# Kernel tuning notes

Measured on AMD Instinct MI355X. Metric: run time of the kernel, lower is better.

## Reference

```python
import jax, jax.numpy as jnp
from jax import lax
import numpy as np

# pywt.Wavelet('sym5').dec_lo; true convolution with rec_lo == correlation with dec_lo
_DEC_LO = jnp.array([0.027333068345077982, 0.029519490925774643, -0.039134249302383094,
                     0.1993975339773936, 0.7234076904024206, 0.6339789634582119,
                     0.01660210576452232, -0.17532808990845047, -0.021101834024758855,
                     0.019538882735286728], dtype=jnp.float32)
_KERNEL = _DEC_LO[None, None, :]  # (O=1, I=1, L=10)


def _idwt_approx(c):
    # One inverse-DWT level with zero detail coeffs.
    # pywt idwt: upsample by 2, full conv with rec_lo, slice [L-2 : L-2 + 2n-L+2].
    # Equivalent: lhs_dilation=2, padding=(1,1), correlation with dec_lo.
    B, n = c.shape
    out = lax.conv_general_dilated(c[:, None, :], _KERNEL, window_strides=(1,),
                                   padding=[(1, 1)], lhs_dilation=(2,),
                                   dimension_numbers=('NCH', 'OIH', 'NCH'))
    return out[:, 0, :]  # (B, 2n - 8)


def _waverec3(cA):
    # waverec with coeffs [cA(20), zeros(20), zeros(31), zeros(54)], sym5 -> length 100
    a = _idwt_approx(cA)      # 20 -> 32
    a = a[:, :31]             # pywt waverec crops a to len(d)=31
    a = _idwt_approx(a)       # 31 -> 54
    a = _idwt_approx(a)       # 54 -> 100
    return a


def _ce(logits, target):
    logp = jax.nn.log_softmax(logits, axis=-1)
    return -jnp.take_along_axis(logp, target[:, None], axis=-1)[:, 0]


def _ohem(logits, target, train_mask, ratio=3.0):
    ce = _ce(logits, target)
    tf = target.astype(jnp.float32)
    pos = (tf * train_mask) > 0
    neg = ((1.0 - tf) * train_mask) > 0
    n_pos = jnp.sum(pos.astype(jnp.float32))
    count_neg = jnp.sum(neg.astype(jnp.float32))
    loss_pos = jnp.where(n_pos > 0, jnp.sum(jnp.where(pos, ce, 0.0)), 0.0)
    n_neg = jnp.where(n_pos > 0, jnp.minimum(count_neg, jnp.floor(ratio * n_pos)), 100.0)
    srt = jnp.sort(jnp.where(neg, ce, -jnp.inf))[::-1]
    take = (jnp.arange(srt.shape[0]) < n_neg) & jnp.isfinite(srt)
    loss_neg = jnp.sum(jnp.where(take, srt, 0.0))
    return (loss_pos + loss_neg) / (n_pos + n_neg)


def _smooth_l1(d):
    ad = jnp.abs(d)
    return jnp.where(ad < 1.0, 0.5 * d * d, ad - 0.5)


def _forward_single(cls_pred, reg_pred, gt):
    cp = jnp.transpose(cls_pred, (0, 2, 3, 1)).reshape(-1, 4)
    rp = jnp.transpose(reg_pred, (0, 2, 3, 1)).reshape(-1, 42)
    g = jnp.transpose(gt, (0, 2, 3, 1)).reshape(-1, 45)
    tr_pred, tcl_pred = cp[:, :2], cp[:, 2:]
    wl_r, xc_p, wl_i, yc_p = rp[:, :20], rp[:, 20], rp[:, 21:41], rp[:, 41]
    tr_mask, tcl_mask, train_mask = g[:, 0], g[:, 1], g[:, 2]
    real_g, xc_g, imag_g, yc_g = g[:, 3:23], g[:, 23], g[:, 24:44], g[:, 44]
    ttm = train_mask * tr_mask
    n_pos = jnp.sum(ttm)

    loss_tr = _ohem(tr_pred, tr_mask.astype(jnp.int32), train_mask)

    ce_tcl = _ce(tcl_pred, tcl_mask.astype(jnp.int32))
    neg_m = 1.0 - ttm
    mp = jnp.sum(ce_tcl * ttm) / jnp.maximum(n_pos, 1.0)
    mn = jnp.sum(ce_tcl * neg_m) / jnp.maximum(jnp.sum(neg_m), 1.0)
    loss_tcl = jnp.where(n_pos > 0, mp + 0.5 * mn, 0.0)

    px = _waverec3(wl_r) + xc_p[:, None]   # (M,100)
    py = _waverec3(wl_i) + yc_p[:, None]
    gx = _waverec3(real_g) + xc_g[:, None]
    gy = _waverec3(imag_g) + yc_g[:, None]
    per_pix = jnp.sum(_smooth_l1(px - gx) + _smooth_l1(py - gy), axis=-1)  # (M,)
    loss_contour = jnp.where(n_pos > 0, 0.5 * jnp.sum(ttm * per_pix) / (n_pos * 200.0), 0.0)
    return jnp.stack([loss_tr, loss_tcl, loss_contour])


def setup_inputs() -> dict:
    key = jax.random.key(0)
    N = 8
    out = {}
    for name, H in (("3", 100), ("4", 50), ("5", 25)):
        k1, k2, k3, k4, k5, k6 = jax.random.split(jax.random.fold_in(key, int(name)), 6)
        out["cls" + name] = jax.random.normal(k1, (N, 4, H, H), jnp.float32)
        out["reg" + name] = jax.random.normal(k2, (N, 42, H, H), jnp.float32)
        tr = jax.random.bernoulli(k3, 0.1, (N, 1, H, H)).astype(jnp.float32)
        tcl = jax.random.bernoulli(k4, 0.5, (N, 1, H, H)).astype(jnp.float32)
        train = jax.random.bernoulli(k5, 0.9, (N, 1, H, H)).astype(jnp.float32)
        rest = jax.random.normal(k6, (N, 42, H, H), jnp.float32)
        out["gt" + name] = jnp.concatenate([tr, tcl, train, rest], axis=1)  # 45 ch
    return out


def reference(cls3, reg3, gt3, cls4, reg4, gt4, cls5, reg5, gt5):
    total = (_forward_single(cls3, reg3, gt3)
             + _forward_single(cls4, reg4, gt4)
             + _forward_single(cls5, reg5, gt5))
    return total  # [loss_text, loss_center, loss_contour]
```

## Files before the change

kernel.cpp:

```cpp
#include <hip/hip_runtime.h>
#include <math.h>

#define DEVI __device__ __forceinline__

static constexpr float KD[10] = {
  0.027333068345077982f,  0.029519490925774643f, -0.039134249302383094f,
  0.1993975339773936f,    0.7234076904024206f,    0.6339789634582119f,
  0.01660210576452232f,  -0.17532808990845047f,  -0.021101834024758855f,
  0.019538882735286728f};

#define CE_OFF     0
#define PH_OFF     105056
#define PH1_REL    40192
#define PH2_REL    50432
#define MH_OFF     160608
#define BS_OFF     234336
#define SLOTGT_OFF 308064
#define STATE_OFF  308352
#define SLOT2_OFF  308384
#define CBUF_OFF   308672
#define CAPC       49152
#define PART_OFF   456128
#define PART_STRIDE 3840

#define NB3 157
#define NB4 40
#define NB5 20
#define NBR 96

DEVI float wave_sum(float v) {
#pragma unroll
  for (int d = 32; d; d >>= 1) v += __shfl_down(v, d);
  return v;
}

DEVI float block_sum(float v, float* sh) {
  int lane = threadIdx.x & 63, wid = threadIdx.x >> 6;
  v = wave_sum(v);
  if (lane == 0) sh[wid] = v;
  __syncthreads();
  if (threadIdx.x == 0) {
    float s = 0.f;
    int nw = blockDim.x >> 6;
    for (int w = 0; w < nw; ++w) s += sh[w];
    sh[0] = s;
  }
  __syncthreads();
  float r = sh[0];
  __syncthreads();
  return r;
}

DEVI int suffix_scan_256(int v, int* sh) {
  int t = threadIdx.x;
  sh[t] = v;
  __syncthreads();
#pragma unroll
  for (int off = 1; off < 256; off <<= 1) {
    int x = (t + off < 256) ? sh[t + off] : 0;
    __syncthreads();
    sh[t] += x;
    __syncthreads();
  }
  return sh[t];
}

DEVI float sl1(float v) { float a = fabsf(v); return (a < 1.f) ? 0.5f * v * v : a - 0.5f; }

DEVI float ce2cls(float la, float lb, float tgt) {
  float m = fmaxf(la, lb);
  float lse = m + __logf(__expf(la - m) + __expf(lb - m));
  return lse - ((tgt > 0.5f) ? lb : la);
}

template <int H>
DEVI float recon_half(const float* __restrict__ rb, const float* __restrict__ gb,
                      int rc0, int gc0, size_t HW, float off) {
  constexpr int CLO  = (H == 0) ? 0 : 6;
  constexpr int A1LO = (H == 0) ? 0 : 12;
  constexpr int J2LO = (H == 0) ? 0 : 25;
  float c[14];
#pragma unroll
  for (int i = 0; i < 14; ++i)
    c[i] = rb[(size_t)(rc0 + CLO + i) * HW] - gb[(size_t)(gc0 + CLO + i) * HW];
  float a1[19];
#pragma unroll
  for (int k = 0; k < 19; ++k) {
    int o1 = A1LO + k, b = (o1 >> 1) - CLO;
    if (o1 & 1)
      a1[k] = KD[0]*c[b] + KD[2]*c[b+1] + KD[4]*c[b+2] + KD[6]*c[b+3] + KD[8]*c[b+4];
    else
      a1[k] = KD[1]*c[b] + KD[3]*c[b+1] + KD[5]*c[b+2] + KD[7]*c[b+3] + KD[9]*c[b+4];
  }
  float w0=0.f,w1=0.f,w2=0.f,w3=0.f,w4=0.f, acc=0.f;
#pragma unroll
  for (int k = 0; k < 29; ++k) {
    int j2 = J2LO + k, b = (j2 >> 1) - A1LO;
    float a2v;
    if (j2 & 1)
      a2v = KD[0]*a1[b] + KD[2]*a1[b+1] + KD[4]*a1[b+2] + KD[6]*a1[b+3] + KD[8]*a1[b+4];
    else
      a2v = KD[1]*a1[b] + KD[3]*a1[b+1] + KD[5]*a1[b+2] + KD[7]*a1[b+3] + KD[9]*a1[b+4];
    w0=w1; w1=w2; w2=w3; w3=w4; w4=a2v;
    if (k >= 4) {
      acc += sl1(KD[1]*w0 + KD[3]*w1 + KD[5]*w2 + KD[7]*w3 + KD[9]*w4 + off);
      acc += sl1(KD[0]*w0 + KD[2]*w1 + KD[4]*w2 + KD[6]*w3 + KD[8]*w4 + off);
    }
  }
  return acc;
}

DEVI float2 tap2o(const float2* a, int b) {
  float2 r;
  r.x = KD[0]*a[b].x + KD[2]*a[b+1].x + KD[4]*a[b+2].x + KD[6]*a[b+3].x + KD[8]*a[b+4].x;
  r.y = KD[0]*a[b].y + KD[2]*a[b+1].y + KD[4]*a[b+2].y + KD[6]*a[b+3].y + KD[8]*a[b+4].y;
  return r;
}
DEVI float2 tap2e(const float2* a, int b) {
  float2 r;
  r.x = KD[1]*a[b].x + KD[3]*a[b+1].x + KD[5]*a[b+2].x + KD[7]*a[b+3].x + KD[9]*a[b+4].x;
  r.y = KD[1]*a[b].y + KD[3]*a[b+1].y + KD[5]*a[b+2].y + KD[7]*a[b+3].y + KD[9]*a[b+4].y;
  return r;
}
template <int H>
DEVI float2 recon2(const float* __restrict__ rb, const float* __restrict__ gb,
                   int rc0, int gc0, size_t HW, float2 off) {
  constexpr int CLO  = (H == 0) ? 0 : 6;
  constexpr int A1LO = (H == 0) ? 0 : 12;
  constexpr int J2LO = (H == 0) ? 0 : 25;
  float2 c[14];
#pragma unroll
  for (int i = 0; i < 14; ++i) {
    float2 rv = *(const float2*)(rb + (size_t)(rc0 + CLO + i) * HW);
    float2 gv = *(const float2*)(gb + (size_t)(gc0 + CLO + i) * HW);
    c[i].x = rv.x - gv.x; c[i].y = rv.y - gv.y;
  }
  float2 a1[19];
#pragma unroll
  for (int k = 0; k < 19; ++k) {
    int o1 = A1LO + k, b = (o1 >> 1) - CLO;
    a1[k] = (o1 & 1) ? tap2o(c, b) : tap2e(c, b);
  }
  float2 w0={0,0},w1={0,0},w2={0,0},w3={0,0},w4={0,0};
  float2 acc={0,0};
#pragma unroll
  for (int k = 0; k < 29; ++k) {
    int j2 = J2LO + k, b = (j2 >> 1) - A1LO;
    float2 a2v = (j2 & 1) ? tap2o(a1, b) : tap2e(a1, b);
    w0=w1; w1=w2; w2=w3; w3=w4; w4=a2v;
    if (k >= 4) {
      float vex = KD[1]*w0.x + KD[3]*w1.x + KD[5]*w2.x + KD[7]*w3.x + KD[9]*w4.x + off.x;
      float vey = KD[1]*w0.y + KD[3]*w1.y + KD[5]*w2.y + KD[7]*w3.y + KD[9]*w4.y + off.y;
      float vox = KD[0]*w0.x + KD[2]*w1.x + KD[4]*w2.x + KD[6]*w3.x + KD[8]*w4.x + off.x;
      float voy = KD[0]*w0.y + KD[2]*w1.y + KD[4]*w2.y + KD[6]*w3.y + KD[8]*w4.y + off.y;
      acc.x += sl1(vex) + sl1(vox);
      acc.y += sl1(vey) + sl1(voy);
    }
  }
  return acc;
}

__global__ void __launch_bounds__(256, 2)
pixel_kernel(const float* __restrict__ cls3, const float* __restrict__ reg3, const float* __restrict__ gt3,
             const float* __restrict__ cls4, const float* __restrict__ reg4, const float* __restrict__ gt4,
             const float* __restrict__ cls5, const float* __restrict__ reg5, const float* __restrict__ gt5,
             float* __restrict__ ws, float* __restrict__ out) {
  int bx = blockIdx.x, y = blockIdx.y, t = threadIdx.x;
  int axis = y >> 1, half = y & 1;
  const float *cls, *reg, *gt;
  int M, HW, ceOff, partBase, phRel, nb, lbx, two;
  if (bx < NB3) {
    cls = cls3; reg = reg3; gt = gt3; M = 80000; HW = 10000;
    ceOff = 0; partBase = PART_OFF; phRel = 0; nb = NB3; lbx = bx; two = 1;
  } else if (bx < NB3 + NB4) {
    cls = cls4; reg = reg4; gt = gt4; M = 20000; HW = 2500;
    ceOff = 80000; partBase = PART_OFF + PART_STRIDE; phRel = PH1_REL; nb = NB4; lbx = bx - NB3; two = 1;
  } else {
    cls = cls5; reg = reg5; gt = gt5; M = 5000; HW = 625;
    ceOff = 100000; partBase = PART_OFF + 2 * PART_STRIDE; phRel = PH2_REL; nb = NB5; lbx = bx - NB3 - NB4; two = 0;
  }
  float* ceArr = ws + ceOff;
  unsigned* ph = (unsigned*)(ws + PH_OFF) + phRel;

  if (bx == 0 && y == 0 && t < 3) out[t] = 0.f;

  __shared__ unsigned hlds[256];
  __shared__ float shp[4][6];
  hlds[t] = 0u;
  __syncthreads();

  float cnt_pos = 0.f, cnt_neg = 0.f, s_ce_pos = 0.f, s_tcl_ttm = 0.f, s_tcl_negm = 0.f;
  float s_ttm_pp = 0.f;
  int rc0 = axis ? 21 : 0;
  int gc0 = axis ? 24 : 3;

  if (two) {
    int p0 = (lbx * 256 + t) * 2;
    if (p0 < M) {
      int n = p0 / HW, hw = p0 % HW;
      const float* gb = gt  + (size_t)n * 45 * HW + hw;
      const float* rb = reg + (size_t)n * 42 * HW + hw;
      float2 trv = *(const float2*)(gb);
      float2 tnv = *(const float2*)(gb + 2 * (size_t)HW);
      float2 ttm; ttm.x = trv.x * tnv.x; ttm.y = trv.y * tnv.y;

      if (y == 0) {
        const float* cb = cls + (size_t)n * 4 * HW + hw;
        float2 l0 = *(const float2*)(cb);
        float2 l1 = *(const float2*)(cb + (size_t)HW);
        float2 l2 = *(const float2*)(cb + 2 * (size_t)HW);
        float2 l3 = *(const float2*)(cb + 3 * (size_t)HW);
        float2 tcl = *(const float2*)(gb + (size_t)HW);
        float cex = ce2cls(l0.x, l1.x, trv.x), cey = ce2cls(l0.y, l1.y, trv.y);
        float ctx = ce2cls(l2.x, l3.x, tcl.x), cty = ce2cls(l2.y, l3.y, tcl.y);
        bool posx = ttm.x > 0.f, posy = ttm.y > 0.f;
        bool negx = ((1.f - trv.x) * tnv.x) > 0.f, negy = ((1.f - trv.y) * tnv.y) > 0.f;
        float cvx = negx ? cex : 0.f, cvy = negy ? cey : 0.f;
        float2 cev; cev.x = cvx; cev.y = cvy;
        *(float2*)(ceArr + p0) = cev;
        if (negx) atomicAdd(&hlds[__float_as_uint(cvx) >> 23], 1u);
        if (negy) atomicAdd(&hlds[__float_as_uint(cvy) >> 23], 1u);
        cnt_pos = (posx ? 1.f : 0.f) + (posy ? 1.f : 0.f);
        cnt_neg = (negx ? 1.f : 0.f) + (negy ? 1.f : 0.f);
        s_ce_pos = (posx ? cex : 0.f) + (posy ? cey : 0.f);
        s_tcl_ttm = ctx * ttm.x + cty * ttm.y;
        s_tcl_negm = ctx * (1.f - ttm.x) + cty * (1.f - ttm.y);
      }

      float2 rcv = *(const float2*)(rb + (size_t)(rc0 + 20) * HW);
      float2 gcv = *(const float2*)(gb + (size_t)(gc0 + 20) * HW);
      float2 dc; dc.x = rcv.x - gcv.x; dc.y = rcv.y - gcv.y;
      float2 pp = half ? recon2<1>(rb, gb, rc0, gc0, (size_t)HW, dc)
                       : recon2<0>(rb, gb, rc0, gc0, (size_t)HW, dc);
      s_ttm_pp = ttm.x * pp.x + ttm.y * pp.y;
    }
  } else {
    int p = lbx * 256 + t;
    if (p < M) {
      int n = p / HW, hw = p % HW;
      const float* gb = gt  + (size_t)n * 45 * HW + hw;
      const float* rb = reg + (size_t)n * 42 * HW + hw;
      float tr = gb[0], train = gb[2 * (size_t)HW];
      float ttm = tr * train;
      if (y == 0) {
        const float* cb = cls + (size_t)n * 4 * HW + hw;
        float ce_tr = ce2cls(cb[0], cb[(size_t)HW], tr);
        float ce_tcl = ce2cls(cb[2 * (size_t)HW], cb[3 * (size_t)HW], gb[(size_t)HW]);
        bool pos = ttm > 0.f;
        bool neg = ((1.f - tr) * train) > 0.f;
        float cev = neg ? ce_tr : 0.f;
        ceArr[p] = cev;
        if (neg) atomicAdd(&hlds[__float_as_uint(cev) >> 23], 1u);
        cnt_pos = pos ? 1.f : 0.f;
        cnt_neg = neg ? 1.f : 0.f;
        s_ce_pos = pos ? ce_tr : 0.f;
        s_tcl_ttm = ce_tcl * ttm;
        s_tcl_negm = ce_tcl * (1.f - ttm);
      }
      float dc = rb[(size_t)(rc0 + 20) * HW] - gb[(size_t)(gc0 + 20) * HW];
      float pp = half ? recon_half<1>(rb, gb, rc0, gc0, (size_t)HW, dc)
                      : recon_half<0>(rb, gb, rc0, gc0, (size_t)HW, dc);
      s_ttm_pp = ttm * pp;
    }
  }

  int lane = t & 63, wid = t >> 6;
  cnt_pos = wave_sum(cnt_pos);
  cnt_neg = wave_sum(cnt_neg);
  s_ce_pos = wave_sum(s_ce_pos);
  s_tcl_ttm = wave_sum(s_tcl_ttm);
  s_tcl_negm = wave_sum(s_tcl_negm);
  s_ttm_pp = wave_sum(s_ttm_pp);
  if (lane == 0) {
    shp[wid][0] = cnt_pos; shp[wid][1] = cnt_neg; shp[wid][2] = s_ce_pos;
    shp[wid][3] = s_tcl_ttm; shp[wid][4] = s_tcl_negm; shp[wid][5] = s_ttm_pp;
  }
  __syncthreads();
  if (t < 6) {
    float s = shp[0][t] + shp[1][t] + shp[2][t] + shp[3][t];
    ws[partBase + (size_t)(y * nb + lbx) * 6 + t] = s;
  }
  if (y == 0)
    ph[(size_t)lbx * 256 + t] = hlds[t];
}

__global__ void refine_kernel(float* __restrict__ ws) {
  int s = blockIdx.y, r = blockIdx.x, t = threadIdx.x;
  int M   = (s == 0) ? 80000 : (s == 1 ? 20000 : 5000);
  int off = (s == 0) ? 0     : (s == 1 ? 80000 : 100000);
  int nb0 = (s == 0) ? NB3   : (s == 1 ? NB4   : NB5);
  int phRel = (s == 0) ? 0 : (s == 1 ? PH1_REL : PH2_REL);
  int* st = (int*)(ws + STATE_OFF) + s * 8;

  __shared__ int sh[256];
  __shared__ int sel[2];
  __shared__ float red[4];
  __shared__ unsigned hW[4][256];
  __shared__ unsigned mhL[256];
  __shared__ float bsL[256];

  const float* part = ws + PART_OFF + s * PART_STRIDE;
  int npart = 4 * nb0;
  float a0 = 0.f, a1 = 0.f, a2 = 0.f, a3 = 0.f, a4 = 0.f, a5 = 0.f;
  for (int i = t; i < npart; i += 256) {
    const float* p6 = part + (size_t)i * 6;
    a0 += p6[0]; a1 += p6[1]; a2 += p6[2]; a3 += p6[3]; a4 += p6[4]; a5 += p6[5];
  }
  a0 = block_sum(a0, red);
  a1 = block_sum(a1, red);
  a2 = block_sum(a2, red);
  a3 = block_sum(a3, red);
  a4 = block_sum(a4, red);
  a5 = block_sum(a5, red);

  float cnt_pos = a0, cnt_negf = a1;
  int cnt_neg = (int)cnt_negf;
  float kf = (cnt_pos > 0.f) ? fminf(cnt_negf, floorf(3.f * cnt_pos)) : 100.f;
  int k_take = min((int)kf, cnt_neg);

  int ibin, rem;
  if (k_take >= cnt_neg) { ibin = -1; rem = 0; }
  else if (k_take <= 0)  { ibin = 256; rem = 0; }
  else {
    const uint4* ph4 = (const uint4*)((const unsigned*)(ws + PH_OFF) + phRel);
    unsigned c0 = 0u, c1 = 0u, c2 = 0u, c3 = 0u;
    int n4 = nb0 * 64;
    for (int i = t; i < n4; i += 256) {
      uint4 u = ph4[i];
      c0 += u.x; c1 += u.y; c2 += u.z; c3 += u.w;
    }
    int wid = t >> 6, b0 = (4 * t) & 255;
    hW[wid][b0 + 0] = c0; hW[wid][b0 + 1] = c1; hW[wid][b0 + 2] = c2; hW[wid][b0 + 3] = c3;
    __syncthreads();
    int h = (int)(hW[0][t] + hW[1][t] + hW[2][t] + hW[3][t]);
    int suf = suffix_scan_256(h, sh);
    int above = suf - h;
    if (suf >= k_take && above < k_take) { sel[0] = t; sel[1] = k_take - above; }
    __syncthreads();
    ibin = sel[0]; rem = sel[1];
    __syncthreads();
  }
  if (r == 0 && t == 0) {
    st[0] = ibin; st[1] = rem;
    float* stf = (float*)st;
    stf[2] = kf; stf[3] = a0; stf[4] = a2; stf[5] = a3; stf[6] = a4; stf[7] = a5;
  }

  mhL[t] = 0u; bsL[t] = 0.f;
  __syncthreads();
  const float* ce = ws + off;
  float sum = 0.f;
  for (int i = r * 256 + t; i < M; i += NBR * 256) {
    float v = ce[i];
    unsigned b = __float_as_uint(v);
    int e = (int)(b >> 23);
    if (e > ibin) sum += v;
    else if (e == ibin && rem > 0) {
      int m8 = (int)((b >> 15) & 255u);
      atomicAdd(&mhL[m8], 1u);
      atomicAdd(&bsL[m8], v);
    }
  }
  sum = block_sum(sum, red);
  if (t == 0) ws[SLOTGT_OFF + s * NBR + r] = sum;
  if (rem > 0) {
    ((unsigned*)(ws + MH_OFF))[((size_t)s * NBR + r) * 256 + t] = mhL[t];
    ws[BS_OFF + ((size_t)s * NBR + r) * 256 + t] = bsL[t];
  }
}

__global__ void compactB_kernel(float* __restrict__ ws) {
  int s = blockIdx.y, r = blockIdx.x, t = threadIdx.x;
  int M   = (s == 0) ? 80000 : (s == 1 ? 20000 : 5000);
  int off = (s == 0) ? 0     : (s == 1 ? 80000 : 100000);
  const int* st = (const int*)(ws + STATE_OFF) + s * 8;
  int ibin = st[0], rem = st[1];
  if (rem <= 0) return;

  __shared__ int sh[256];
  __shared__ int sel[2];
  __shared__ float red[4];
  __shared__ unsigned hW[4][256];
  __shared__ unsigned wcnt;

  const unsigned* mh = (const unsigned*)(ws + MH_OFF) + (size_t)s * NBR * 256;
  const uint4* mh4 = (const uint4*)mh;
  unsigned c0 = 0u, c1 = 0u, c2 = 0u, c3 = 0u;
  for (int i = t; i < NBR * 64; i += 256) {
    uint4 u = mh4[i];
    c0 += u.x; c1 += u.y; c2 += u.z; c3 += u.w;
  }
  int wid = t >> 6, b0 = (4 * t) & 255;
  hW[wid][b0 + 0] = c0; hW[wid][b0 + 1] = c1; hW[wid][b0 + 2] = c2; hW[wid][b0 + 3] = c3;
  __syncthreads();
  int h = (int)(hW[0][t] + hW[1][t] + hW[2][t] + hW[3][t]);
  int suf = suffix_scan_256(h, sh);
  int above = suf - h;
  if (suf >= rem && above < rem) { sel[0] = t; }
  __syncthreads();
  int jbin = sel[0];
  __syncthreads();

  float v2 = ws[BS_OFF + ((size_t)s * NBR + r) * 256 + t];
  float gt2 = block_sum((t > jbin) ? v2 : 0.f, red);
  if (t == 0) ws[SLOT2_OFF + s * NBR + r] = gt2;

  int cval = (t < NBR) ? (int)mh[(size_t)t * 256 + jbin] : 0;
  sh[t] = cval;
  __syncthreads();
#pragma unroll
  for (int o = 1; o < 128; o <<= 1) {
    int x = (t >= o) ? sh[t - o] : 0;
    __syncthreads();
    sh[t] += x;
    __syncthreads();
  }
  int base = (r > 0) ? sh[r - 1] : 0;

  if (t == 0) wcnt = 0u;
  __syncthreads();
  const float* ce = ws + off;
  float* cbuf = ws + CBUF_OFF + (size_t)s * CAPC;
  for (int i = r * 256 + t; i < M; i += NBR * 256) {
    float v = ce[i];
    unsigned b = __float_as_uint(v);
    if ((int)(b >> 23) == ibin && (int)((b >> 15) & 255u) == jbin) {
      unsigned idx = (unsigned)base + atomicAdd(&wcnt, 1u);
      if (idx < CAPC) cbuf[idx] = v;
    }
  }
}

__global__ void final_kernel(float* __restrict__ ws, float* __restrict__ out) {
  int s = blockIdx.x, t = threadIdx.x;
  int M = (s == 0) ? 80000 : (s == 1 ? 20000 : 5000);
  const int* st = (const int*)(ws + STATE_OFF) + s * 8;
  const float* stf = (const float*)st;

  __shared__ int sh[256];
  __shared__ int sel[2];
  __shared__ float red[4];
  __shared__ unsigned hW[4][256];
  __shared__ int hist[256];

  int ibin = st[0], rem = st[1];
  float kf = stf[2], n_pos = stf[3];
  float s_ce_pos = stf[4], s_tcl_ttm = stf[5], s_tcl_negm = stf[6], s_ttm_pp = stf[7];

  float lpart = (t < NBR) ? ws[SLOTGT_OFF + s * NBR + t] : 0.f;
  float loss_neg = block_sum(lpart, red);

  if (rem > 0) {
    const uint4* mh4 = (const uint4*)((const unsigned*)(ws + MH_OFF) + (size_t)s * NBR * 256);
    unsigned c0 = 0u, c1 = 0u, c2 = 0u, c3 = 0u;
    for (int i = t; i < NBR * 64; i += 256) {
      uint4 u = mh4[i];
      c0 += u.x; c1 += u.y; c2 += u.z; c3 += u.w;
    }
    int wid = t >> 6, b0 = (4 * t) & 255;
    hW[wid][b0 + 0] = c0; hW[wid][b0 + 1] = c1; hW[wid][b0 + 2] = c2; hW[wid][b0 + 3] = c3;
    __syncthreads();
    int h = (int)(hW[0][t] + hW[1][t] + hW[2][t] + hW[3][t]);
    int suf = suffix_scan_256(h, sh);
    int above = suf - h;
    if (suf >= rem && above < rem) { sel[0] = t; sel[1] = rem - above; }
    __syncthreads();
    int jbin = sel[0], rem2 = sel[1];
    int jcnt = (int)(hW[0][jbin] + hW[1][jbin] + hW[2][jbin] + hW[3][jbin]);
    __syncthreads();

    float l2 = (t < NBR) ? ws[SLOT2_OFF + s * NBR + t] : 0.f;
    loss_neg += block_sum(l2, red);

    int cnt = min(jcnt, CAPC);
    const float* cbuf = ws + CBUF_OFF + (size_t)s * CAPC;

    hist[t] = 0; __syncthreads();
    for (int i = t; i < cnt; i += 256)
      atomicAdd(&hist[(__float_as_uint(cbuf[i]) >> 7) & 255u], 1);
    __syncthreads();
    h = hist[t];
    suf = suffix_scan_256(h, sh);
    above = suf - h;
    int remcur = rem2;
    if (suf >= remcur && above < remcur) { sel[0] = t; sel[1] = remcur - above; }
    __syncthreads();
    int b1 = sel[0]; remcur = sel[1];
    __syncthreads();

    hist[t] = 0; __syncthreads();
    for (int i = t; i < cnt; i += 256) {
      unsigned b = __float_as_uint(cbuf[i]);
      if (((b >> 7) & 255u) == (unsigned)b1) atomicAdd(&hist[b & 127u], 1);
    }
    __syncthreads();
    h = (t < 128) ? hist[t] : 0;
    suf = suffix_scan_256(h, sh);
    above = suf - h;
    if (t < 128 && suf >= remcur && above < remcur) { sel[0] = t; }
    __syncthreads();
    int lb0 = sel[0];
    __syncthreads();

    unsigned prefix = ((unsigned)ibin << 23) | ((unsigned)jbin << 15) |
                      ((unsigned)b1 << 7) | (unsigned)lb0;
    float tval = __uint_as_float(prefix);

    float sum_in = 0.f, cgt = 0.f;
    for (int i = t; i < cnt; i += 256) {
      unsigned b = __float_as_uint(cbuf[i]);
      if (b > prefix) { sum_in += cbuf[i]; cgt += 1.f; }
    }
    sum_in = block_sum(sum_in, red);
    cgt = block_sum(cgt, red);
    loss_neg += sum_in + ((float)rem2 - cgt) * tval;
  }

  if (t == 0) {
    float loss_pos = (n_pos > 0.f) ? s_ce_pos : 0.f;
    float loss_tr = (loss_pos + loss_neg) / (n_pos + kf);

    float negm = (float)M - n_pos;
    float mp = s_tcl_ttm / fmaxf(n_pos, 1.f);
    float mn = s_tcl_negm / fmaxf(negm, 1.f);
    float loss_tcl = (n_pos > 0.f) ? (mp + 0.5f * mn) : 0.f;

    float loss_ct = (n_pos > 0.f) ? (0.5f * s_ttm_pp / (n_pos * 200.f)) : 0.f;

    atomicAdd(&out[0], loss_tr);
    atomicAdd(&out[1], loss_tcl);
    atomicAdd(&out[2], loss_ct);
  }
}

extern "C" void kernel_launch(void* const* d_in, const int* in_sizes, int n_in,
                              void* d_out, int out_size, void* d_ws, size_t ws_size,
                              hipStream_t stream) {
  (void)in_sizes; (void)n_in; (void)out_size; (void)ws_size;
  const float* cls3 = (const float*)d_in[0];
  const float* reg3 = (const float*)d_in[1];
  const float* gt3  = (const float*)d_in[2];
  const float* cls4 = (const float*)d_in[3];
  const float* reg4 = (const float*)d_in[4];
  const float* gt4  = (const float*)d_in[5];
  const float* cls5 = (const float*)d_in[6];
  const float* reg5 = (const float*)d_in[7];
  const float* gt5  = (const float*)d_in[8];

  float* ws = (float*)d_ws;
  float* out = (float*)d_out;

  pixel_kernel<<<dim3(NB3 + NB4 + NB5, 4), 256, 0, stream>>>(
      cls3, reg3, gt3, cls4, reg4, gt4, cls5, reg5, gt5, ws, out);

  refine_kernel<<<dim3(NBR, 3), 256, 0, stream>>>(ws);
  compactB_kernel<<<dim3(NBR, 3), 256, 0, stream>>>(ws);
  final_kernel<<<3, 256, 0, stream>>>(ws, out);
}
```

Baseline: 58.58 us.

## Fuse final reduction into compaction kernel via last-block ticket; halve pixel block size

Merges final_kernel into compactB_kernel: each block bumps a per-scale ticket counter after compaction, and the last block to arrive runs the final top-k selection and loss. This drops one kernel launch and its dependency gap. Separately, the pixel kernel moves from 256-thread to 128-thread blocks, roughly doubling the block count and reworking the workspace offsets, which should spread the work across more CUs. The trade-offs are extra threadfence and atomic overhead, and more per-block histogram partials for refine to read.

```diff
diff --git a/kernel.cpp b/kernel.cpp
--- a/kernel.cpp
+++ b/kernel.cpp
@@ -11,21 +11,22 @@
 
 #define CE_OFF     0
 #define PH_OFF     105056
-#define PH1_REL    40192
-#define PH2_REL    50432
-#define MH_OFF     160608
-#define BS_OFF     234336
-#define SLOTGT_OFF 308064
-#define STATE_OFF  308352
-#define SLOT2_OFF  308384
-#define CBUF_OFF   308672
+#define PH1_REL    80128
+#define PH2_REL    100352
+#define MH_OFF     215648
+#define BS_OFF     289376
+#define SLOTGT_OFF 363104
+#define STATE_OFF  363392
+#define SLOT2_OFF  363424
+#define TICKET_OFF 363712
+#define CBUF_OFF   363728
 #define CAPC       49152
-#define PART_OFF   456128
-#define PART_STRIDE 3840
-
-#define NB3 157
-#define NB4 40
-#define NB5 20
+#define PART_OFF   511200
+#define PART_STRIDE 7680
+
+#define NB3 313
+#define NB4 79
+#define NB5 40
 #define NBR 96
 
 DEVI float wave_sum(float v) {
@@ -160,7 +161,7 @@
   return acc;
 }
 
-__global__ void __launch_bounds__(256, 2)
+__global__ void __launch_bounds__(128, 3)
 pixel_kernel(const float* __restrict__ cls3, const float* __restrict__ reg3, const float* __restrict__ gt3,
              const float* __restrict__ cls4, const float* __restrict__ reg4, const float* __restrict__ gt4,
              const float* __restrict__ cls5, const float* __restrict__ reg5, const float* __restrict__ gt5,
@@ -185,8 +186,8 @@
   if (bx == 0 && y == 0 && t < 3) out[t] = 0.f;
 
   __shared__ unsigned hlds[256];
-  __shared__ float shp[4][6];
-  hlds[t] = 0u;
+  __shared__ float shp[2][6];
+  hlds[t] = 0u; hlds[t + 128] = 0u;
   __syncthreads();
 
   float cnt_pos = 0.f, cnt_neg = 0.f, s_ce_pos = 0.f, s_tcl_ttm = 0.f, s_tcl_negm = 0.f;
@@ -195,7 +196,7 @@
   int gc0 = axis ? 24 : 3;
 
   if (two) {
-    int p0 = (lbx * 256 + t) * 2;
+    int p0 = (lbx * 128 + t) * 2;
     if (p0 < M) {
       int n = p0 / HW, hw = p0 % HW;
       const float* gb = gt  + (size_t)n * 45 * HW + hw;
@@ -235,7 +236,7 @@
       s_ttm_pp = ttm.x * pp.x + ttm.y * pp.y;
     }
   } else {
-    int p = lbx * 256 + t;
+    int p = lbx * 128 + t;
     if (p < M) {
       int n = p / HW, hw = p % HW;
       const float* gb = gt  + (size_t)n * 45 * HW + hw;
@@ -277,11 +278,13 @@
   }
   __syncthreads();
   if (t < 6) {
-    float s = shp[0][t] + shp[1][t] + shp[2][t] + shp[3][t];
+    float s = shp[0][t] + shp[1][t];
     ws[partBase + (size_t)(y * nb + lbx) * 6 + t] = s;
   }
-  if (y == 0)
+  if (y == 0) {
     ph[(size_t)lbx * 256 + t] = hlds[t];
+    ph[(size_t)lbx * 256 + t + 128] = hlds[t + 128];
+  }
 }
 
 __global__ void refine_kernel(float* __restrict__ ws) {
@@ -291,6 +294,8 @@
   int nb0 = (s == 0) ? NB3   : (s == 1 ? NB4   : NB5);
   int phRel = (s == 0) ? 0 : (s == 1 ? PH1_REL : PH2_REL);
   int* st = (int*)(ws + STATE_OFF) + s * 8;
+
+  if (r == 0 && t == 0) ((unsigned*)(ws + TICKET_OFF))[s] = 0u;
 
   __shared__ int sh[256];
   __shared__ int sel[2];
@@ -369,89 +374,26 @@
   }
 }
 
-__global__ void compactB_kernel(float* __restrict__ ws) {
+__global__ void compactB_kernel(float* __restrict__ ws, float* __restrict__ out) {
   int s = blockIdx.y, r = blockIdx.x, t = threadIdx.x;
   int M   = (s == 0) ? 80000 : (s == 1 ? 20000 : 5000);
   int off = (s == 0) ? 0     : (s == 1 ? 80000 : 100000);
   const int* st = (const int*)(ws + STATE_OFF) + s * 8;
+  const float* stf = (const float*)st;
   int ibin = st[0], rem = st[1];
-  if (rem <= 0) return;
-
-  __shared__ int sh[256];
-  __shared__ int sel[2];
-  __shared__ float red[4];
-  __shared__ unsigned hW[4][256];
-  __shared__ unsigned wcnt;
-
-  const unsigned* mh = (const unsigned*)(ws + MH_OFF) + (size_t)s * NBR * 256;
-  const uint4* mh4 = (const uint4*)mh;
-  unsigned c0 = 0u, c1 = 0u, c2 = 0u, c3 = 0u;
-  for (int i = t; i < NBR * 64; i += 256) {
-    uint4 u = mh4[i];
-    c0 += u.x; c1 += u.y; c2 += u.z; c3 += u.w;
-  }
-  int wid = t >> 6, b0 = (4 * t) & 255;
-  hW[wid][b0 + 0] = c0; hW[wid][b0 + 1] = c1; hW[wid][b0 + 2] = c2; hW[wid][b0 + 3] = c3;
-  __syncthreads();
-  int h = (int)(hW[0][t] + hW[1][t] + hW[2][t] + hW[3][t]);
-  int suf = suffix_scan_256(h, sh);
-  int above = suf - h;
-  if (suf >= rem && above < rem) { sel[0] = t; }
-  __syncthreads();
-  int jbin = sel[0];
-  __syncthreads();
-
-  float v2 = ws[BS_OFF + ((size_t)s * NBR + r) * 256 + t];
-  float gt2 = block_sum((t > jbin) ? v2 : 0.f, red);
-  if (t == 0) ws[SLOT2_OFF + s * NBR + r] = gt2;
-
-  int cval = (t < NBR) ? (int)mh[(size_t)t * 256 + jbin] : 0;
-  sh[t] = cval;
-  __syncthreads();
-#pragma unroll
-  for (int o = 1; o < 128; o <<= 1) {
-    int x = (t >= o) ? sh[t - o] : 0;
-    __syncthreads();
-    sh[t] += x;
-    __syncthreads();
-  }
-  int base = (r > 0) ? sh[r - 1] : 0;
-
-  if (t == 0) wcnt = 0u;
-  __syncthreads();
-  const float* ce = ws + off;
-  float* cbuf = ws + CBUF_OFF + (size_t)s * CAPC;
-  for (int i = r * 256 + t; i < M; i += NBR * 256) {
-    float v = ce[i];
-    unsigned b = __float_as_uint(v);
-    if ((int)(b >> 23) == ibin && (int)((b >> 15) & 255u) == jbin) {
-      unsigned idx = (unsigned)base + atomicAdd(&wcnt, 1u);
-      if (idx < CAPC) cbuf[idx] = v;
-    }
-  }
-}
-
-__global__ void final_kernel(float* __restrict__ ws, float* __restrict__ out) {
-  int s = blockIdx.x, t = threadIdx.x;
-  int M = (s == 0) ? 80000 : (s == 1 ? 20000 : 5000);
-  const int* st = (const int*)(ws + STATE_OFF) + s * 8;
-  const float* stf = (const float*)st;
 
   __shared__ int sh[256];
   __shared__ int sel[2];
   __shared__ float red[4];
   __shared__ unsigned hW[4][256];
   __shared__ int hist[256];
-
-  int ibin = st[0], rem = st[1];
-  float kf = stf[2], n_pos = stf[3];
-  float s_ce_pos = stf[4], s_tcl_ttm = stf[5], s_tcl_negm = stf[6], s_ttm_pp = stf[7];
-
-  float lpart = (t < NBR) ? ws[SLOTGT_OFF + s * NBR + t] : 0.f;
-  float loss_neg = block_sum(lpart, red);
-
+  __shared__ unsigned wcnt;
+  __shared__ unsigned tickL;
+
+  int jbin = 0, rem2 = 0, jcnt = 0;
   if (rem > 0) {
-    const uint4* mh4 = (const uint4*)((const unsigned*)(ws + MH_OFF) + (size_t)s * NBR * 256);
+    const unsigned* mh = (const unsigned*)(ws + MH_OFF) + (size_t)s * NBR * 256;
+    const uint4* mh4 = (const uint4*)mh;
     unsigned c0 = 0u, c1 = 0u, c2 = 0u, c3 = 0u;
     for (int i = t; i < NBR * 64; i += 256) {
       uint4 u = mh4[i];
@@ -465,10 +407,54 @@
     int above = suf - h;
     if (suf >= rem && above < rem) { sel[0] = t; sel[1] = rem - above; }
     __syncthreads();
-    int jbin = sel[0], rem2 = sel[1];
-    int jcnt = (int)(hW[0][jbin] + hW[1][jbin] + hW[2][jbin] + hW[3][jbin]);
-    __syncthreads();
-
+    jbin = sel[0]; rem2 = sel[1];
+    jcnt = (int)(hW[0][jbin] + hW[1][jbin] + hW[2][jbin] + hW[3][jbin]);
+    __syncthreads();
+
+    float v2 = ws[BS_OFF + ((size_t)s * NBR + r) * 256 + t];
+    float gt2 = block_sum((t > jbin) ? v2 : 0.f, red);
+    if (t == 0) ws[SLOT2_OFF + s * NBR + r] = gt2;
+
+    int cval = (t < NBR) ? (int)mh[(size_t)t * 256 + jbin] : 0;
+    sh[t] = cval;
+    __syncthreads();
+#pragma unroll
+    for (int o = 1; o < 128; o <<= 1) {
+      int x = (t >= o) ? sh[t - o] : 0;
+      __syncthreads();
+      sh[t] += x;
+      __syncthreads();
+    }
+    int base = (r > 0) ? sh[r - 1] : 0;
+
+    if (t == 0) wcnt = 0u;
+    __syncthreads();
+    const float* ce = ws + off;
+    float* cbuf = ws + CBUF_OFF + (size_t)s * CAPC;
+    for (int i = r * 256 + t; i < M; i += NBR * 256) {
+      float v = ce[i];
+      unsigned b = __float_as_uint(v);
+      if ((int)(b >> 23) == ibin && (int)((b >> 15) & 255u) == jbin) {
+        unsigned idx = (unsigned)base + atomicAdd(&wcnt, 1u);
+        if (idx < CAPC) cbuf[idx] = v;
+      }
+    }
+  }
+
+  __threadfence();
+  __syncthreads();
+  if (t == 0) tickL = atomicAdd(&((unsigned*)(ws + TICKET_OFF))[s], 1u);
+  __syncthreads();
+  if (tickL != (unsigned)(NBR - 1)) return;
+  __threadfence();
+
+  float kf = stf[2], n_pos = stf[3];
+  float s_ce_pos = stf[4], s_tcl_ttm = stf[5], s_tcl_negm = stf[6], s_ttm_pp = stf[7];
+
+  float lpart = (t < NBR) ? ws[SLOTGT_OFF + s * NBR + t] : 0.f;
+  float loss_neg = block_sum(lpart, red);
+
+  if (rem > 0) {
     float l2 = (t < NBR) ? ws[SLOT2_OFF + s * NBR + t] : 0.f;
     loss_neg += block_sum(l2, red);
 
@@ -479,9 +465,9 @@
     for (int i = t; i < cnt; i += 256)
       atomicAdd(&hist[(__float_as_uint(cbuf[i]) >> 7) & 255u], 1);
     __syncthreads();
-    h = hist[t];
-    suf = suffix_scan_256(h, sh);
-    above = suf - h;
+    int h = hist[t];
+    int suf = suffix_scan_256(h, sh);
+    int above = suf - h;
     int remcur = rem2;
     if (suf >= remcur && above < remcur) { sel[0] = t; sel[1] = remcur - above; }
     __syncthreads();
@@ -550,10 +536,9 @@
   float* ws = (float*)d_ws;
   float* out = (float*)d_out;
 
-  pixel_kernel<<<dim3(NB3 + NB4 + NB5, 4), 256, 0, stream>>>(
+  pixel_kernel<<<dim3(NB3 + NB4 + NB5, 4), 128, 0, stream>>>(
       cls3, reg3, gt3, cls4, reg4, gt4, cls5, reg5, gt5, ws, out);
 
   refine_kernel<<<dim3(NBR, 3), 256, 0, stream>>>(ws);
-  compactB_kernel<<<dim3(NBR, 3), 256, 0, stream>>>(ws);
-  final_kernel<<<3, 256, 0, stream>>>(ws, out);
-}
+  compactB_kernel<<<dim3(NBR, 3), 256, 0, stream>>>(ws, out);
+}
```

Measured after the change: 79.65 us. +36.0%, slower.
